# Optimization experiments

Measured on AMD Instinct MI355X. Metric: run time of the kernel, lower is better.

## Reference

```python
import jax, jax.numpy as jnp
import numpy as np

TAU = 1.0  # initial_temperature, non-trainable
EPS = 1e-10


def setup_inputs() -> dict:
    key = jax.random.key(0)
    ks = jax.random.split(key, 5)
    B, D, E, A = 8192, 1024, 32, 128
    x = jax.random.normal(ks[0], (B, D), dtype=jnp.float32)
    W_att = jax.random.normal(ks[1], (E, D), dtype=jnp.float32) * (1.0 / np.sqrt(D))
    b_att = jnp.zeros((E,), dtype=jnp.float32)
    adaptive_bias = jnp.zeros((E,), dtype=jnp.float32)
    W_strat = jax.random.normal(ks[2], (E, A, D), dtype=jnp.float32) * (1.0 / np.sqrt(D))
    b_strat = jnp.zeros((E, A), dtype=jnp.float32)
    gumbel_u = jax.random.uniform(ks[3], (B, E), dtype=jnp.float32)
    return {"x": x, "W_att": W_att, "b_att": b_att, "adaptive_bias": adaptive_bias,
            "W_strat": W_strat, "b_strat": b_strat, "gumbel_u": gumbel_u}


def reference(x, W_att, b_att, adaptive_bias, W_strat, b_strat, gumbel_u):
    # Gating: linear + adaptive bias, then gumbel-softmax with temperature TAU
    logits = x @ W_att.T + b_att + adaptive_bias            # [B, E]
    g = -jnp.log(-jnp.log(gumbel_u + EPS) + EPS)            # gumbel noise [B, E]
    weights = jax.nn.softmax((logits + g) / TAU, axis=-1)   # [B, E] soft selection
    # Per-strategy outputs: each strategy is Linear(D -> A)
    strat_out = jnp.einsum('bd,ead->bea', x, W_strat) + b_strat  # [B, E, A]
    # Weighted combine (superposition)
    out = jnp.einsum('be,bea->ba', weights, strat_out)      # [B, A]
    return out
```

## Files before the change

kernel.cpp:

```cpp
#include <hip/hip_runtime.h>
#include <stdint.h>

typedef unsigned short u16;
typedef __attribute__((ext_vector_type(4))) float f32x4;
typedef __attribute__((ext_vector_type(8))) short short8;
typedef __attribute__((ext_vector_type(8))) unsigned short u16x8;

static constexpr int Bq = 8192;
static constexpr int Dq = 1024;
static constexpr int Eq = 32;
static constexpr int Aq = 128;
static constexpr int NSTRAT = 4096;

__device__ inline u16 f32_to_bf16_rne(float f) {
    uint32_t u = __float_as_uint(f);
    uint32_t r = 0x7fffu + ((u >> 16) & 1u);
    return (u16)((u + r) >> 16);
}
__device__ inline float bf16_to_f32(u16 h) {
    return __uint_as_float(((uint32_t)h) << 16);
}
__device__ inline void gload_lds16(const u16* g, u16* l) {
    __builtin_amdgcn_global_load_lds(
        (const __attribute__((address_space(1))) void*)g,
        (__attribute__((address_space(3))) void*)l, 16, 0, 0);
}
__device__ inline short8 cvt8(const float* p) {
    f32x4 a = *(const f32x4*)p;
    f32x4 b = *(const f32x4*)(p + 4);
    short8 o;
    o[0] = (short)f32_to_bf16_rne(a[0]); o[1] = (short)f32_to_bf16_rne(a[1]);
    o[2] = (short)f32_to_bf16_rne(a[2]); o[3] = (short)f32_to_bf16_rne(a[3]);
    o[4] = (short)f32_to_bf16_rne(b[0]); o[5] = (short)f32_to_bf16_rne(b[1]);
    o[6] = (short)f32_to_bf16_rne(b[2]); o[7] = (short)f32_to_bf16_rne(b[3]);
    return o;
}
template <int CTRL>
__device__ inline float dppadd(float v) {
    int t = __builtin_amdgcn_update_dpp(0, __float_as_int(v), CTRL, 0xf, 0xf, false);
    return v + __int_as_float(t);
}
__device__ inline float red16(float v) {
    v = dppadd<0xb1>(v);
    v = dppadd<0x4e>(v);
    v = dppadd<0x124>(v);
    v = dppadd<0x128>(v);
    return v;
}

#define MF(a, b, c) __builtin_amdgcn_mfma_f32_16x16x32_bf16(a, b, c, 0, 0, 0)

__global__ __launch_bounds__(256) void cvt_fused(const float* __restrict__ x,
                                                 const float* __restrict__ Ws,
                                                 u16* __restrict__ xb) {
    size_t i = ((size_t)blockIdx.x * 256 + threadIdx.x) * 8;
    const size_t XN = (size_t)Bq * Dq;
    const float* src;
    if (i < XN) {
        src = x + i;
    } else {
        size_t j = i - XN;
        int rp = (int)(j >> 10);
        int e = rp & 31;
        int a = rp >> 5;
        src = Ws + ((size_t)((e << 7) + a) << 10) + (j & 1023);
    }
    short8 o = cvt8(src);
    *(short8*)(xb + i) = o;
}

__global__ __launch_bounds__(512) void logits_kernel(const u16* __restrict__ xb,
                                                     const float* __restrict__ W_att,
                                                     const float* __restrict__ b_att,
                                                     const float* __restrict__ abias,
                                                     const float* __restrict__ gu,
                                                     float* __restrict__ wT) {
    __shared__ __align__(16) u16 Wa[32][1032];

    const int tid = threadIdx.x;
    const int lane = tid & 63;
    const int wv = tid >> 6;
    const int fr = lane & 15;
    const int fq = lane >> 4;
    const int m0 = blockIdx.x * 128;

    {
        const int row = tid >> 4;
        const int col0 = (tid & 15) * 64;
        const float* src = W_att + (size_t)row * 1024 + col0;
        u16* dst = &Wa[row][col0];
#pragma unroll
        for (int it = 0; it < 8; ++it) {
            short8 o = cvt8(src + it * 8);
            *(short8*)(dst + it * 8) = o;
        }
    }
    __syncthreads();

    f32x4 acc0 = {}, acc1 = {};
    const u16* xrow = xb + (size_t)(m0 + wv * 16 + fr) * 1024 + fq * 8;
#pragma unroll 4
    for (int k0 = 0; k0 < 1024; k0 += 32) {
        short8 a0 = *(const short8*)(xrow + k0);
        short8 b0 = *(const short8*)(&Wa[fr][k0 + fq * 8]);
        short8 b1 = *(const short8*)(&Wa[16 + fr][k0 + fq * 8]);
        acc0 = MF(a0, b0, acc0);
        acc1 = MF(a0, b1, acc1);
    }

    const float bba0 = b_att[fr] + abias[fr];
    const float bba1 = b_att[16 + fr] + abias[16 + fr];
#pragma unroll
    for (int q = 0; q < 4; ++q) {
        const int row = m0 + wv * 16 + fq * 4 + q;
        float u0 = gu[(size_t)row * 32 + fr];
        float u1 = gu[(size_t)row * 32 + 16 + fr];
        float g0 = -logf(-logf(u0 + 1e-10f) + 1e-10f);
        float g1 = -logf(-logf(u1 + 1e-10f) + 1e-10f);
        float z0 = acc0[q] + bba0 + g0;
        float z1 = acc1[q] + bba1 + g1;
        float mx = fmaxf(z0, z1);
#pragma unroll
        for (int s = 1; s < 16; s <<= 1) mx = fmaxf(mx, __shfl_xor(mx, s));
        float p0 = __expf(z0 - mx);
        float p1 = __expf(z1 - mx);
        float sm = p0 + p1;
#pragma unroll
        for (int s = 1; s < 16; s <<= 1) sm += __shfl_xor(sm, s);
        float inv = 1.0f / sm;
        wT[(size_t)fr * Bq + row] = p0 * inv;
        wT[(size_t)(16 + fr) * Bq + row] = p1 * inv;
    }
}

#define FBAR do { asm volatile("" ::: "memory"); __builtin_amdgcn_s_barrier(); asm volatile("" ::: "memory"); } while (0)
#define LGKM0 asm volatile("s_waitcnt lgkmcnt(0)" ::: "memory")
#define VMCNT(n) asm volatile("s_waitcnt vmcnt(" #n ")" ::: "memory")
#define SB __builtin_amdgcn_sched_barrier(0)
#define PRIO1 __builtin_amdgcn_s_setprio(1)
#define PRIO0 __builtin_amdgcn_s_setprio(0)


#define STAGE_A(buf, h, kt) do { \
    gload_lds16(agA + (size_t)((h)*128) * 1024 + (size_t)(kt) * 64, (u16*)&lds[buf][h][tid * 8]); \
    gload_lds16(agA + (size_t)((h)*128 + 64) * 1024 + (size_t)(kt) * 64, (u16*)&lds[buf][h][4096 + tid * 8]); \
} while (0)
#define STAGE_B(buf, h, kt) do { \
    gload_lds16(agB + (size_t)((h)*128) * 1024 + (size_t)(kt) * 64, (u16*)&lds[buf][2 + (h)][tid * 8]); \
    gload_lds16(agB + (size_t)((h)*128 + 64) * 1024 + (size_t)(kt) * 64, (u16*)&lds[buf][2 + (h)][4096 + tid * 8]); \
} while (0)

#define LDA8(DST, ABASE, mq) do { \
    DST[0] = *(const short8*)((ABASE) + (mq)*4096 + 0*1024 + aoff0); \
    DST[1] = *(const short8*)((ABASE) + (mq)*4096 + 0*1024 + aoff1); \
    DST[2] = *(const short8*)((ABASE) + (mq)*4096 + 1*1024 + aoff0); \
    DST[3] = *(const short8*)((ABASE) + (mq)*4096 + 1*1024 + aoff1); \
    DST[4] = *(const short8*)((ABASE) + (mq)*4096 + 2*1024 + aoff0); \
    DST[5] = *(const short8*)((ABASE) + (mq)*4096 + 2*1024 + aoff1); \
    DST[6] = *(const short8*)((ABASE) + (mq)*4096 + 3*1024 + aoff0); \
    DST[7] = *(const short8*)((ABASE) + (mq)*4096 + 3*1024 + aoff1); \
} while (0)
#define LDB4(DST, BBASE, nq) do { \
    DST[0] = *(const short8*)((BBASE) + (nq)*2048 + 0*1024 + boff0); \
    DST[1] = *(const short8*)((BBASE) + (nq)*2048 + 0*1024 + boff1); \
    DST[2] = *(const short8*)((BBASE) + (nq)*2048 + 1*1024 + boff0); \
    DST[3] = *(const short8*)((BBASE) + (nq)*2048 + 1*1024 + boff1); \
} while (0)

#define QUAD(mq, nq, AS, BS) do { \
    acc[(mq)*4+0][(nq)*2+0] = MF(AS[0], BS[0], acc[(mq)*4+0][(nq)*2+0]); \
    acc[(mq)*4+0][(nq)*2+1] = MF(AS[0], BS[2], acc[(mq)*4+0][(nq)*2+1]); \
    acc[(mq)*4+1][(nq)*2+0] = MF(AS[2], BS[0], acc[(mq)*4+1][(nq)*2+0]); \
    acc[(mq)*4+1][(nq)*2+1] = MF(AS[2], BS[2], acc[(mq)*4+1][(nq)*2+1]); \
    acc[(mq)*4+2][(nq)*2+0] = MF(AS[4], BS[0], acc[(mq)*4+2][(nq)*2+0]); \
    acc[(mq)*4+2][(nq)*2+1] = MF(AS[4], BS[2], acc[(mq)*4+2][(nq)*2+1]); \
    acc[(mq)*4+3][(nq)*2+0] = MF(AS[6], BS[0], acc[(mq)*4+3][(nq)*2+0]); \
    acc[(mq)*4+3][(nq)*2+1] = MF(AS[6], BS[2], acc[(mq)*4+3][(nq)*2+1]); \
    acc[(mq)*4+0][(nq)*2+0] = MF(AS[1], BS[1], acc[(mq)*4+0][(nq)*2+0]); \
    acc[(mq)*4+0][(nq)*2+1] = MF(AS[1], BS[3], acc[(mq)*4+0][(nq)*2+1]); \
    acc[(mq)*4+1][(nq)*2+0] = MF(AS[3], BS[1], acc[(mq)*4+1][(nq)*2+0]); \
    acc[(mq)*4+1][(nq)*2+1] = MF(AS[3], BS[3], acc[(mq)*4+1][(nq)*2+1]); \
    acc[(mq)*4+2][(nq)*2+0] = MF(AS[5], BS[1], acc[(mq)*4+2][(nq)*2+0]); \
    acc[(mq)*4+2][(nq)*2+1] = MF(AS[5], BS[3], acc[(mq)*4+2][(nq)*2+1]); \
    acc[(mq)*4+3][(nq)*2+0] = MF(AS[7], BS[1], acc[(mq)*4+3][(nq)*2+0]); \
    acc[(mq)*4+3][(nq)*2+1] = MF(AS[7], BS[3], acc[(mq)*4+3][(nq)*2+1]); \
} while (0)

#define GITER(t, TAIL) do { \
     \
    LDB4(Bs0, Bbase0, 0); \
    STAGE_A(1, 0, (t) + 1); \
    SB; FBAR; LGKM0; SB; \
    PRIO1; QUAD(0, 0, As0, Bs0); PRIO0; SB; FBAR; \
     \
    LDB4(Bs1, Bbase0, 1); \
    STAGE_A(1, 1, (t) + 1); \
    SB; FBAR; LGKM0; SB; \
    PRIO1; QUAD(0, 1, As0, Bs1); PRIO0; SB; FBAR; \
     \
    LDA8(As1, Abase0, 1); \
    if (!(TAIL)) STAGE_B(0, 0, (t) + 2); \
    SB; FBAR; LGKM0; SB; \
    PRIO1; QUAD(1, 1, As1, Bs1); PRIO0; SB; \
    if (TAIL) { VMCNT(0); } else { VMCNT(2); } \
    FBAR; \
     \
    LDA8(As0, Abase1, 0); \
    if (!(TAIL)) STAGE_B(0, 1, (t) + 2); \
    SB; FBAR; LGKM0; SB; \
    PRIO1; QUAD(1, 0, As1, Bs0); PRIO0; SB; FBAR; \
     \
    LDB4(Bs0, Bbase1, 0); \
    if (!(TAIL)) STAGE_A(0, 0, (t) + 2); \
    SB; FBAR; LGKM0; SB; \
    PRIO1; QUAD(0, 0, As0, Bs0); PRIO0; SB; FBAR; \
     \
    LDB4(Bs1, Bbase1, 1); \
    if (!(TAIL)) STAGE_A(0, 1, (t) + 2); \
    SB; FBAR; LGKM0; SB; \
    PRIO1; QUAD(0, 1, As0, Bs1); PRIO0; SB; FBAR; \
     \
    LDA8(As1, Abase1, 1); \
    if (!(TAIL)) STAGE_B(1, 0, (t) + 3); \
    SB; FBAR; LGKM0; SB; \
    PRIO1; QUAD(1, 1, As1, Bs1); PRIO0; SB; \
    if (!(TAIL)) { VMCNT(2); } \
    FBAR; \
     \
    if (!(TAIL)) { LDA8(As0, Abase0, 0); STAGE_B(1, 1, (t) + 3); } \
    SB; FBAR; LGKM0; SB; \
    PRIO1; QUAD(1, 0, As1, Bs0); PRIO0; SB; FBAR; \
} while (0)

__global__ __launch_bounds__(512, 2) void gemm256(const u16* __restrict__ Abuf,
                                                  const u16* __restrict__ Bbuf,
                                                  const float* __restrict__ wT,
                                                  const float* __restrict__ b_strat,
                                                  float* __restrict__ out) {
    __shared__ __align__(16) u16 lds[2][4][8192];

    const int tid = threadIdx.x;
    const int lane = tid & 63;
    const int wv = tid >> 6;
    const int wr = wv >> 2;
    const int wc = wv & 3;
    const int fr = lane & 15;
    const int fq = lane >> 4;

    const int bid = blockIdx.x;
    const int xcd = bid & 7;
    const int k = bid >> 3;
    const int m0 = (xcd * 4 + (k & 3)) * 256;
    const int n0 = (k >> 2) * 256;

    const int s_r = tid >> 3;
    const int s_c = ((tid & 7) * 8) ^ ((s_r & 7) << 3);
    const u16* agA = Abuf + (size_t)(m0 + s_r) * 1024 + s_c;
    const u16* agB = Bbuf + (size_t)(n0 + s_r) * 1024 + s_c;

    const int aoff0 = fr * 64 + ((fq ^ (fr & 7)) * 8);
    const int aoff1 = fr * 64 + (((fq + 4) ^ (fr & 7)) * 8);
    const int bof = (wc & 1) * 4096;
    const int boff0 = bof + aoff0;
    const int boff1 = bof + aoff1;

    const u16* Abase0 = (const u16*)&lds[0][wr][0];
    const u16* Abase1 = (const u16*)&lds[1][wr][0];
    const u16* Bbase0 = (const u16*)&lds[0][2 + (wc >> 1)][0];
    const u16* Bbase1 = (const u16*)&lds[1][2 + (wc >> 1)][0];

    f32x4 acc[8][4] = {};
    short8 As0[8], As1[8], Bs0[4], Bs1[4];

    STAGE_A(0, 0, 0); STAGE_A(0, 1, 0); STAGE_B(0, 0, 0); STAGE_B(0, 1, 0);
    STAGE_B(1, 0, 1); STAGE_B(1, 1, 1);
    SB; VMCNT(4); FBAR;
    LDA8(As0, Abase0, 0);

#pragma unroll 1
    for (int t = 0; t < 14; t += 2) { GITER(t, 0); }
    GITER(14, 1);

    const int crow = m0 + wr * 128 + fq * 4;
    const int a0 = (n0 >> 5) + wc * 2;
    const float bs00 = b_strat[fr * 128 + a0];
    const float bs10 = b_strat[(16 + fr) * 128 + a0];
    const float bs01 = b_strat[fr * 128 + a0 + 1];
    const float bs11 = b_strat[(16 + fr) * 128 + a0 + 1];
    const float* wt0 = wT + (size_t)fr * Bq;
    const float* wt1 = wT + (size_t)(16 + fr) * Bq;
#pragma unroll
    for (int im = 0; im < 8; ++im) {
        f32x4 w0 = *(const f32x4*)(wt0 + crow + im * 16);
        f32x4 w1 = *(const f32x4*)(wt1 + crow + im * 16);
#pragma unroll
        for (int q = 0; q < 4; ++q) {
            float v0 = w0[q] * (acc[im][0][q] + bs00) + w1[q] * (acc[im][1][q] + bs10);
            float v1 = w0[q] * (acc[im][2][q] + bs01) + w1[q] * (acc[im][3][q] + bs11);
            v0 = red16(v0);
            v1 = red16(v1);
            if (fr == 0) {
                const int row = crow + im * 16 + q;
                out[(size_t)row * 128 + a0] = v0;
                out[(size_t)row * 128 + a0 + 1] = v1;
            }
        }
    }
}

extern "C" void kernel_launch(void* const* d_in, const int* in_sizes, int n_in,
                              void* d_out, int out_size, void* d_ws, size_t ws_size,
                              hipStream_t stream) {
    (void)in_sizes; (void)n_in; (void)out_size; (void)ws_size;
    const float* x       = (const float*)d_in[0];
    const float* W_att   = (const float*)d_in[1];
    const float* b_att   = (const float*)d_in[2];
    const float* abias   = (const float*)d_in[3];
    const float* W_strat = (const float*)d_in[4];
    const float* b_strat = (const float*)d_in[5];
    const float* gu      = (const float*)d_in[6];
    float* out = (float*)d_out;

    u16* xb = (u16*)d_ws;
    u16* Wb = xb + (size_t)Bq * Dq;
    float* wT = (float*)(Wb + (size_t)NSTRAT * Dq);

    cvt_fused<<<(Bq * Dq + NSTRAT * Dq) / (256 * 8), 256, 0, stream>>>(x, W_strat, xb);

    logits_kernel<<<Bq / 128, 512, 0, stream>>>(xb, W_att, b_att, abias, gu, wT);

    gemm256<<<512, 512, 0, stream>>>(xb, Wb, wT, b_strat, out);
}
```

Baseline: 92.87 us.

## Process two N tiles per block, prefetching next tile during epilogue

Each GEMM block now computes two consecutive 256-wide N tiles in sequence, halving the grid to 256 blocks. The next tile's first K stages are issued before the epilogue of the current tile, so the global-to-LDS loads overlap the weighted-reduction stores. The aim is to hide pipeline ramp-up and epilogue latency behind each other. In exchange, only 256 blocks run, which may leave CUs underused on a 256-CU part and removes the slack from a second wave of blocks.

```diff
diff --git a/kernel.cpp b/kernel.cpp
--- a/kernel.cpp
+++ b/kernel.cpp
@@ -141,14 +141,16 @@
 #define PRIO0 __builtin_amdgcn_s_setprio(0)
 
 
-#define STAGE_A(buf, h, kt) do { \
-    gload_lds16(agA + (size_t)((h)*128) * 1024 + (size_t)(kt) * 64, (u16*)&lds[buf][h][tid * 8]); \
-    gload_lds16(agA + (size_t)((h)*128 + 64) * 1024 + (size_t)(kt) * 64, (u16*)&lds[buf][h][4096 + tid * 8]); \
-} while (0)
-#define STAGE_B(buf, h, kt) do { \
-    gload_lds16(agB + (size_t)((h)*128) * 1024 + (size_t)(kt) * 64, (u16*)&lds[buf][2 + (h)][tid * 8]); \
-    gload_lds16(agB + (size_t)((h)*128 + 64) * 1024 + (size_t)(kt) * 64, (u16*)&lds[buf][2 + (h)][4096 + tid * 8]); \
-} while (0)
+#define STAGE_AP(gp, buf, h, kt) do { \
+    gload_lds16((gp) + (size_t)((h)*128) * 1024 + (size_t)(kt) * 64, (u16*)&lds[buf][h][tid * 8]); \
+    gload_lds16((gp) + (size_t)((h)*128 + 64) * 1024 + (size_t)(kt) * 64, (u16*)&lds[buf][h][4096 + tid * 8]); \
+} while (0)
+#define STAGE_BP(gp, buf, h, kt) do { \
+    gload_lds16((gp) + (size_t)((h)*128) * 1024 + (size_t)(kt) * 64, (u16*)&lds[buf][2 + (h)][tid * 8]); \
+    gload_lds16((gp) + (size_t)((h)*128 + 64) * 1024 + (size_t)(kt) * 64, (u16*)&lds[buf][2 + (h)][4096 + tid * 8]); \
+} while (0)
+#define STAGE_A(buf, h, kt) STAGE_AP(agA, buf, h, kt)
+#define STAGE_B(buf, h, kt) STAGE_BP(agB, buf, h, kt)
 
 #define LDA8(DST, ABASE, mq) do { \
     DST[0] = *(const short8*)((ABASE) + (mq)*4096 + 0*1024 + aoff0); \
@@ -251,7 +253,7 @@
     const int xcd = bid & 7;
     const int k = bid >> 3;
     const int m0 = (xcd * 4 + (k & 3)) * 256;
-    const int n0 = (k >> 2) * 256;
+    const int n0 = (k >> 2) * 512;
 
     const int s_r = tid >> 3;
     const int s_c = ((tid & 7) * 8) ^ ((s_r & 7) << 3);
@@ -272,38 +274,63 @@
     f32x4 acc[8][4] = {};
     short8 As0[8], As1[8], Bs0[4], Bs1[4];
 
+    const int crow = m0 + wr * 128 + fq * 4;
+    const float* wt0 = wT + (size_t)fr * Bq;
+    const float* wt1 = wT + (size_t)(16 + fr) * Bq;
+
     STAGE_A(0, 0, 0); STAGE_A(0, 1, 0); STAGE_B(0, 0, 0); STAGE_B(0, 1, 0);
     STAGE_B(1, 0, 1); STAGE_B(1, 1, 1);
     SB; VMCNT(4); FBAR;
     LDA8(As0, Abase0, 0);
 
 #pragma unroll 1
-    for (int t = 0; t < 14; t += 2) { GITER(t, 0); }
-    GITER(14, 1);
-
-    const int crow = m0 + wr * 128 + fq * 4;
-    const int a0 = (n0 >> 5) + wc * 2;
-    const float bs00 = b_strat[fr * 128 + a0];
-    const float bs10 = b_strat[(16 + fr) * 128 + a0];
-    const float bs01 = b_strat[fr * 128 + a0 + 1];
-    const float bs11 = b_strat[(16 + fr) * 128 + a0 + 1];
-    const float* wt0 = wT + (size_t)fr * Bq;
-    const float* wt1 = wT + (size_t)(16 + fr) * Bq;
-#pragma unroll
-    for (int im = 0; im < 8; ++im) {
-        f32x4 w0 = *(const f32x4*)(wt0 + crow + im * 16);
-        f32x4 w1 = *(const f32x4*)(wt1 + crow + im * 16);
-#pragma unroll
-        for (int q = 0; q < 4; ++q) {
-            float v0 = w0[q] * (acc[im][0][q] + bs00) + w1[q] * (acc[im][1][q] + bs10);
-            float v1 = w0[q] * (acc[im][2][q] + bs01) + w1[q] * (acc[im][3][q] + bs11);
-            v0 = red16(v0);
-            v1 = red16(v1);
-            if (fr == 0) {
-                const int row = crow + im * 16 + q;
-                out[(size_t)row * 128 + a0] = v0;
-                out[(size_t)row * 128 + a0 + 1] = v1;
+    for (int rep = 0; rep < 2; ++rep) {
+#pragma unroll 1
+        for (int t = 0; t < 14; t += 2) { GITER(t, 0); }
+        GITER(14, 1);
+
+        if (rep == 0) {
+            const u16* agBn = agB + 256 * 1024;
+            STAGE_AP(agA, 0, 0, 0); STAGE_AP(agA, 0, 1, 0);
+            STAGE_BP(agBn, 0, 0, 0); STAGE_BP(agBn, 0, 1, 0);
+            STAGE_BP(agBn, 1, 0, 1); STAGE_BP(agBn, 1, 1, 1);
+        }
+
+        {
+            const int n0r = n0 + rep * 256;
+            const int a0 = (n0r >> 5) + wc * 2;
+            const float bs00 = b_strat[fr * 128 + a0];
+            const float bs10 = b_strat[(16 + fr) * 128 + a0];
+            const float bs01 = b_strat[fr * 128 + a0 + 1];
+            const float bs11 = b_strat[(16 + fr) * 128 + a0 + 1];
+#pragma unroll
+            for (int im = 0; im < 8; ++im) {
+                f32x4 w0 = *(const f32x4*)(wt0 + crow + im * 16);
+                f32x4 w1 = *(const f32x4*)(wt1 + crow + im * 16);
+#pragma unroll
+                for (int q = 0; q < 4; ++q) {
+                    float v0 = w0[q] * (acc[im][0][q] + bs00) + w1[q] * (acc[im][1][q] + bs10);
+                    float v1 = w0[q] * (acc[im][2][q] + bs01) + w1[q] * (acc[im][3][q] + bs11);
+                    v0 = red16(v0);
+                    v1 = red16(v1);
+                    if (fr == 0) {
+                        const int row = crow + im * 16 + q;
+                        out[(size_t)row * 128 + a0] = v0;
+                        out[(size_t)row * 128 + a0 + 1] = v1;
+                    }
+                }
             }
+        }
+
+        if (rep == 0) {
+#pragma unroll
+            for (int im = 0; im < 8; ++im)
+#pragma unroll
+                for (int jn = 0; jn < 4; ++jn)
+                    acc[im][jn] = (f32x4){0.f, 0.f, 0.f, 0.f};
+            agB += 256 * 1024;
+            SB; VMCNT(4); FBAR;
+            LDA8(As0, Abase0, 0);
         }
     }
 }
@@ -329,5 +356,5 @@
 
     logits_kernel<<<Bq / 128, 512, 0, stream>>>(xb, W_att, b_att, abias, gu, wT);
 
-    gemm256<<<512, 512, 0, stream>>>(xb, Wb, wT, b_strat, out);
-}
+    gemm256<<<256, 512, 0, stream>>>(xb, Wb, wT, b_strat, out);
+}
```

After: 98.07 us. 1.06x slower.
